# Optimization experiments

Hardware: AMD Instinct MI355X
Metric: run time of the kernel (lower is better)

## Reference

```python
import jax, jax.numpy as jnp
import numpy as np

N_NODES, N_EDGES, N_GRAPHS, NUM_FEATURES, NUM_CLASSES = 100000, 1600000, 512, 128, 10
EPS = 1e-5


def gat_conv(x, W, a_src, a_dst, b, src, dst, heads, out_ch):
    # PyG GATConv: h = xW -> [N,H,C]; per-node scores; leaky_relu; segment softmax over dst; scatter-add
    N = x.shape[0]
    h = (x @ W).reshape(N, heads, out_ch)
    s_src = jnp.einsum('nhc,hc->nh', h, a_src)
    s_dst = jnp.einsum('nhc,hc->nh', h, a_dst)
    score = jax.nn.leaky_relu(s_src[src] + s_dst[dst], 0.2)          # [E,H]
    m = jax.ops.segment_max(score, dst, num_segments=N)              # stable softmax per dst node
    e = jnp.exp(score - m[dst])
    denom = jax.ops.segment_sum(e, dst, num_segments=N)
    alpha = e / denom[dst]                                            # self-loops guarantee denom>0
    out = jax.ops.segment_sum(alpha[:, :, None] * h[src], dst, num_segments=N)
    return out.reshape(N, heads * out_ch) + b


def batch_norm(x, g, b):
    mu = x.mean(0)
    var = x.var(0)  # biased, as torch BN uses for normalization
    return g * (x - mu) * jax.lax.rsqrt(var + EPS) + b


def setup_inputs() -> dict:
    key = jax.random.key(0)
    ks = jax.random.split(key, 32)
    r = lambda i, shape: jax.random.normal(ks[i], shape, dtype=jnp.float32) * 0.1
    inp = {
        'x': jax.random.normal(ks[0], (N_NODES, NUM_FEATURES), dtype=jnp.float32),
        'edge_index': jax.random.randint(ks[1], (2, N_EDGES), 0, N_NODES, dtype=jnp.int64),
        'batch': jnp.sort(jax.random.randint(ks[2], (N_NODES,), 0, N_GRAPHS, dtype=jnp.int64)),
        # conv1: 128 -> 8 ch x 8 heads
        'W1': r(3, (NUM_FEATURES, 64)), 'a1s': r(4, (8, 8)), 'a1d': r(5, (8, 8)), 'b1': r(6, (64,)),
        'g1': jnp.ones(64), 'be1': jnp.zeros(64),
        'lW1': r(7, (64, 8)), 'lb1': r(8, (8,)), 'gl1': jnp.ones(8), 'bel1': jnp.zeros(8),
        # conv2: 8 -> 16 ch x 4 heads
        'W2': r(9, (8, 64)), 'a2s': r(10, (4, 16)), 'a2d': r(11, (4, 16)), 'b2': r(12, (64,)),
        'g2': jnp.ones(64), 'be2': jnp.zeros(64),
        'lW2': r(13, (64, 16)), 'lb2': r(14, (16,)), 'gl2': jnp.ones(16), 'bel2': jnp.zeros(16),
        # conv3: 16 -> 24 ch x 4 heads
        'W3': r(15, (16, 96)), 'a3s': r(16, (4, 24)), 'a3d': r(17, (4, 24)), 'b3': r(18, (96,)),
        'g3': jnp.ones(96), 'be3': jnp.zeros(96),
        'oW': r(19, (96, NUM_CLASSES)), 'ob': r(20, (NUM_CLASSES,)),
    }
    return inp


def reference(x, edge_index, batch, W1, a1s, a1d, b1, g1, be1, lW1, lb1, gl1, bel1,
              W2, a2s, a2d, b2, g2, be2, lW2, lb2, gl2, bel2,
              W3, a3s, a3d, b3, g3, be3, oW, ob):
    N = x.shape[0]
    loops = jnp.arange(N, dtype=edge_index.dtype)
    src = jnp.concatenate([edge_index[0], loops])  # PyG add_self_loops default
    dst = jnp.concatenate([edge_index[1], loops])

    h = gat_conv(x, W1, a1s, a1d, b1, src, dst, 8, 8)
    h = jax.nn.relu(batch_norm(h, g1, be1))
    h = jax.nn.relu(batch_norm(h @ lW1 + lb1, gl1, bel1))

    h = gat_conv(h, W2, a2s, a2d, b2, src, dst, 4, 16)
    h = jax.nn.relu(batch_norm(h, g2, be2))
    h = jax.nn.relu(batch_norm(h @ lW2 + lb2, gl2, bel2))

    h = gat_conv(h, W3, a3s, a3d, b3, src, dst, 4, 24)
    h = jax.nn.relu(batch_norm(h, g3, be3))

    sums = jax.ops.segment_sum(h, batch, num_segments=N_GRAPHS)
    cnts = jax.ops.segment_sum(jnp.ones((N,), h.dtype), batch, num_segments=N_GRAPHS)
    pooled = sums / jnp.maximum(cnts, 1.0)[:, None]
    return pooled @ oW + ob
```

## Files before the change

kernel.cpp:

```cpp
#include <hip/hip_runtime.h>
#include <hip/hip_fp16.h>
#include <math.h>

#define NN 100000
#define NE 1600000
#define ET (NE + NN)
#define NG 512
#define STATS_BLOCKS 240
#define SCAN_B 1024
#define SCAN_NB ((NN + SCAN_B - 1) / SCAN_B)
#define PSLOTS (ET + 7 * NN)

#define BSH 9
#define NB  ((NN + 511) / 512)
#define BCAP 12288
#define CHUNK 4096


__global__ __launch_bounds__(256) void part_pass1(const int* __restrict__ ei,
                                                  int* __restrict__ bcur,
                                                  unsigned* __restrict__ pairs) {
    __shared__ unsigned pck[CHUNK];
    __shared__ unsigned ordv[CHUNK];
    __shared__ unsigned char bkt[CHUNK];
    __shared__ unsigned char obkt[CHUNK];
    __shared__ int hist[NB + 1];
    __shared__ int lofs[NB + 1];
    __shared__ int cur[NB + 1];
    __shared__ int gpos[NB];
    __shared__ int lh[256];

    int t = threadIdx.x;
    int base = blockIdx.x * CHUNK;
    for (int i = t; i <= NB; i += 256) hist[i] = 0;
    __syncthreads();
    for (int i = t; i < CHUNK; i += 256) {
        int e = base + i;
        int b;
        unsigned p = 0;
        if (e < ET) {
            int s, d;
            if (e < NE) { s = ei[e]; d = ei[NE + e]; }
            else        { s = d = e - NE; }
            b = d >> BSH;
            p = ((unsigned)s << BSH) | (unsigned)(d & 511);
        } else b = NB;
        bkt[i] = (unsigned char)b;
        pck[i] = p;
        atomicAdd(&hist[b], 1);
    }
    __syncthreads();
    int v = (t <= NB) ? hist[t] : 0;
    lh[t] = v;
    __syncthreads();
    for (int off = 1; off < 256; off <<= 1) {
        int x = (t >= off) ? lh[t - off] : 0;
        __syncthreads();
        lh[t] += x;
        __syncthreads();
    }
    if (t <= NB) { lofs[t] = lh[t] - v; cur[t] = lh[t] - v; }
    __syncthreads();
    if (t < NB) {
        int h = hist[t];
        gpos[t] = (h > 0) ? atomicAdd(&bcur[t], h) : 0;
    }
    __syncthreads();
    for (int i = t; i < CHUNK; i += 256) {
        int b = bkt[i];
        int pos = atomicAdd(&cur[b], 1);
        ordv[pos] = pck[i];
        obkt[pos] = (unsigned char)b;
    }
    __syncthreads();
    int nvalid = lofs[NB];
    for (int i = t; i < nvalid; i += 256) {
        int b = obkt[i];
        int dst = gpos[b] + (i - lofs[b]);
        if (dst < BCAP) pairs[(size_t)b * BCAP + dst] = ordv[i];
    }
}


__global__ __launch_bounds__(256) void bucket_counts(const unsigned* __restrict__ pairs,
                                                     const int* __restrict__ bcur,
                                                     int* __restrict__ counts) {
    __shared__ int lhist[512];
    int b = blockIdx.x;
    int t = threadIdx.x;
    for (int i = t; i < 512; i += 256) lhist[i] = 0;
    __syncthreads();
    int cnt = min(bcur[b], BCAP);
    const unsigned* seg = pairs + (size_t)b * BCAP;
    for (int i = t; i < cnt; i += 256)
        atomicAdd(&lhist[seg[i] & 511], 1);
    __syncthreads();
    int nbase = b << BSH;
    for (int i = t; i < 512; i += 256) {
        int n = nbase + i;
        if (n < NN) counts[n] = lhist[i];
    }
}


__global__ __launch_bounds__(256) void bucket_scatter(const unsigned* __restrict__ pairs,
                                                      const int* __restrict__ bcur,
                                                      const int* __restrict__ offsets,
                                                      int* __restrict__ srcs) {
    __shared__ int cur[512];
    int b = blockIdx.x;
    int t = threadIdx.x;
    int nbase = b << BSH;
    for (int i = t; i < 512; i += 256) {
        int n = nbase + i;
        cur[i] = (n < NN) ? offsets[n] : 0;
    }
    __syncthreads();
    int cnt = min(bcur[b], BCAP);
    const unsigned* seg = pairs + (size_t)b * BCAP;
    for (int i = t; i < cnt; i += 256) {
        unsigned p = seg[i];
        int pos = atomicAdd(&cur[p & 511], 1);
        srcs[pos] = (int)(p >> BSH);
    }
}


__global__ void graph_bounds(const int* __restrict__ batch, int* __restrict__ goff) {
    int g = blockIdx.x * blockDim.x + threadIdx.x;
    if (g > NG) return;
    int lo = 0, hi = NN;
    while (lo < hi) {
        int mid = (lo + hi) >> 1;
        if (batch[mid] < g) lo = mid + 1; else hi = mid;
    }
    goff[g] = lo;
}


__global__ void scan_reduce(const int* __restrict__ in, int* __restrict__ bsum) {
    __shared__ int lds[256];
    int b = blockIdx.x, t = threadIdx.x;
    int s = 0;
    for (int i = t; i < SCAN_B; i += 256) {
        int idx = b * SCAN_B + i;
        if (idx < NN) s += (in[idx] + 7) & ~7;
    }
    lds[t] = s;
    __syncthreads();
    for (int off = 128; off > 0; off >>= 1) {
        if (t < off) lds[t] += lds[t + off];
        __syncthreads();
    }
    if (t == 0) bsum[b] = lds[0];
}

__global__ void scan_bsums(const int* __restrict__ bsum, int nb, int* __restrict__ boff,
                           int* __restrict__ total_loc) {
    __shared__ int lds[128];
    int t = threadIdx.x;
    int v = (t < nb) ? bsum[t] : 0;
    lds[t] = v;
    __syncthreads();
    for (int off = 1; off < 128; off <<= 1) {
        int x = (t >= off) ? lds[t - off] : 0;
        __syncthreads();
        lds[t] += x;
        __syncthreads();
    }
    if (t < nb) boff[t] = lds[t] - v;
    if (t == nb - 1) {
        boff[nb] = lds[t];
        if (total_loc) *total_loc = lds[t];
    }
}

__global__ void scan_final(const int* __restrict__ in, const int* __restrict__ boff,
                           int* __restrict__ out) {
    __shared__ int lds[SCAN_B];
    int b = blockIdx.x, t = threadIdx.x;
    int idx = b * SCAN_B + t;
    int v = (idx < NN) ? ((in[idx] + 7) & ~7) : 0;
    lds[t] = v;
    __syncthreads();
    for (int off = 1; off < SCAN_B; off <<= 1) {
        int x = (t >= off) ? lds[t - off] : 0;
        __syncthreads();
        lds[t] += x;
        __syncthreads();
    }
    if (idx < NN) out[idx] = boff[b] + lds[t] - v;
}


__global__ __launch_bounds__(256) void gemm1(const float* __restrict__ X,
                                             const float* __restrict__ W,
                                             const float* __restrict__ a_s,
                                             const float* __restrict__ a_d,
                                             __half* __restrict__ Hh,
                                             float* __restrict__ SS,
                                             float* __restrict__ SD) {
    __shared__ float wl[128 * 64];
    __shared__ float xl[32 * 132];
    int t = threadIdx.x;
    int n0 = blockIdx.x * 32;
    for (int i = t * 4; i < 128 * 64; i += 1024)
        *(float4*)&wl[i] = *(const float4*)&W[i];
    for (int i = t * 4; i < 32 * 128; i += 1024) {
        int r = i >> 7, c = i & 127;
        int n = n0 + r;
        float4 v = (n < NN) ? *(const float4*)&X[(size_t)n * 128 + c] : make_float4(0, 0, 0, 0);
        *(float4*)&xl[r * 132 + c] = v;
    }
    __syncthreads();
    int cg = (t & 15) * 4;
    int ng = (t >> 4) * 2;
    float acc[2][4] = {};
    for (int k = 0; k < 128; ++k) {
        float4 w4 = *(float4*)&wl[k * 64 + cg];
        #pragma unroll
        for (int j = 0; j < 2; ++j) {
            float xv = xl[(ng + j) * 132 + k];
            acc[j][0] += xv * w4.x; acc[j][1] += xv * w4.y;
            acc[j][2] += xv * w4.z; acc[j][3] += xv * w4.w;
        }
    }
    int hd = cg >> 3;
    int half = cg & 7;
    #pragma unroll
    for (int j = 0; j < 2; ++j) {
        int n = n0 + ng + j;
        float p1 = 0.f, p2 = 0.f;
        #pragma unroll
        for (int k = 0; k < 4; ++k) {
            p1 += acc[j][k] * a_s[hd * 8 + half + k];
            p2 += acc[j][k] * a_d[hd * 8 + half + k];
        }
        float f1 = p1 + __shfl_xor(p1, 1, 64);
        float f2 = p2 + __shfl_xor(p2, 1, 64);
        if (n < NN) {
            __half2 q0 = __floats2half2_rn(acc[j][0], acc[j][1]);
            __half2 q1 = __floats2half2_rn(acc[j][2], acc[j][3]);
            *(__half2*)&Hh[(size_t)n * 64 + cg] = q0;
            *(__half2*)&Hh[(size_t)n * 64 + cg + 2] = q1;
            if (half == 0) {
                SS[(unsigned)n * 8 + hd] = f1;
                SD[(unsigned)n * 8 + hd] = f2;
            }
        }
    }
}


template <int HEADS, int C, int PL, int GRP>
__global__ __launch_bounds__(256) void gat_kernel(const __half* __restrict__ Hh,
                                                  const float* __restrict__ SS,
                                                  const float* __restrict__ SD,
                                                  const int* __restrict__ offsets,
                                                  const int* __restrict__ counts,
                                                  const int* __restrict__ srcs,
                                                  const float* __restrict__ bias,
                                                  __half* __restrict__ GO) {
    constexpr int CH = HEADS * C;
    int wid = blockIdx.x * (blockDim.x >> 6) + (threadIdx.x >> 6);
    int lane = threadIdx.x & 63;
    if (wid >= NN) return;
    int ch0 = lane * PL;
    bool active = ch0 < CH;
    int ch0l = active ? ch0 : 0;
    int head = active ? (ch0 / C) : 0;
    int beg = offsets[wid], end = offsets[wid + 1];
    int deg = counts[wid];
    float sdv = SD[(unsigned)wid * HEADS + head];
    float s = 0.f, a0 = 0.f, a1 = 0.f;
    int e = beg;
    if (GRP == 16) {
        for (; e + 16 <= end; e += 16) {
            int sv[16];
            float wv[16];
            #pragma unroll
            for (int i = 0; i < 16; ++i) {
                sv[i] = srcs[e + i];
                float sc = SS[(unsigned)(sv[i] * HEADS) + head] + sdv;
                sc = fmaxf(sc, 0.f) + 0.2f * fminf(sc, 0.f);
                wv[i] = (e + i - beg) < deg ? __expf(sc) : 0.f;
            }
            float hv0[16];
            #pragma unroll
            for (int i = 0; i < 16; ++i)
                hv0[i] = __half2float(Hh[(unsigned)(sv[i] * CH) + ch0l]);
            float pw[8], pa[8];
            #pragma unroll
            for (int i = 0; i < 8; ++i) {
                pw[i] = wv[2 * i] + wv[2 * i + 1];
                pa[i] = wv[2 * i] * hv0[2 * i] + wv[2 * i + 1] * hv0[2 * i + 1];
            }
            s  += ((pw[0] + pw[1]) + (pw[2] + pw[3])) + ((pw[4] + pw[5]) + (pw[6] + pw[7]));
            a0 += ((pa[0] + pa[1]) + (pa[2] + pa[3])) + ((pa[4] + pa[5]) + (pa[6] + pa[7]));
        }
    }
    for (; e < end; e += 8) {
        int sv[8];
        float wv[8];
        #pragma unroll
        for (int i = 0; i < 8; ++i) {
            sv[i] = srcs[e + i];
            float sc = SS[(unsigned)(sv[i] * HEADS) + head] + sdv;
            sc = fmaxf(sc, 0.f) + 0.2f * fminf(sc, 0.f);
            wv[i] = (e + i - beg) < deg ? __expf(sc) : 0.f;
        }
        float hv0[8], hv1[8];
        #pragma unroll
        for (int i = 0; i < 8; ++i) {
            if (PL == 2) {
                __half2 hp = *(const __half2*)&Hh[(unsigned)(sv[i] * CH) + ch0l];
                hv0[i] = __low2float(hp); hv1[i] = __high2float(hp);
            } else {
                hv0[i] = __half2float(Hh[(unsigned)(sv[i] * CH) + ch0l]);
                hv1[i] = 0.f;
            }
        }
        float ws = ((wv[0] + wv[1]) + (wv[2] + wv[3])) + ((wv[4] + wv[5]) + (wv[6] + wv[7]));
        float as0 = ((wv[0] * hv0[0] + wv[1] * hv0[1]) + (wv[2] * hv0[2] + wv[3] * hv0[3]))
                  + ((wv[4] * hv0[4] + wv[5] * hv0[5]) + (wv[6] * hv0[6] + wv[7] * hv0[7]));
        s += ws;
        a0 += as0;
        if (PL == 2) {
            float as1 = ((wv[0] * hv1[0] + wv[1] * hv1[1]) + (wv[2] * hv1[2] + wv[3] * hv1[3]))
                      + ((wv[4] * hv1[4] + wv[5] * hv1[5]) + (wv[6] * hv1[6] + wv[7] * hv1[7]));
            a1 += as1;
        }
    }
    if (active) {
        float inv = 1.f / s;
        if (PL == 2) {
            *(__half2*)&GO[(unsigned)(wid * CH) + ch0] =
                __floats2half2_rn(a0 * inv + bias[ch0], a1 * inv + bias[ch0 + 1]);
        } else {
            GO[(unsigned)(wid * CH) + ch0] = __float2half(a0 * inv + bias[ch0]);
        }
    }
}


__global__ void stats_kernel(const float* __restrict__ X, int Nn, int C,
                             float* __restrict__ partial) {
    int t = threadIdx.x;
    int c = t % C;
    int grp = t / C;
    int G_ = blockDim.x / C;
    float s = 0.f, q = 0.f;
    for (int n = blockIdx.x * G_ + grp; n < Nn; n += gridDim.x * G_) {
        float v = X[(size_t)n * C + c];
        s += v; q += v * v;
    }
    extern __shared__ float lds[];
    lds[t] = s; lds[blockDim.x + t] = q;
    __syncthreads();
    for (int off = blockDim.x >> 1; off >= C; off >>= 1) {
        if (t < off) {
            lds[t] += lds[t + off];
            lds[blockDim.x + t] += lds[blockDim.x + t + off];
        }
        __syncthreads();
    }
    if (t < C) {
        partial[(size_t)blockIdx.x * 2 * C + t] = lds[t];
        partial[(size_t)blockIdx.x * 2 * C + C + t] = lds[blockDim.x + t];
    }
}

__global__ void stats_h_kernel(const __half* __restrict__ X, int Nn, int C,
                               float* __restrict__ partial) {
    int t = threadIdx.x;
    int c = t % C;
    int grp = t / C;
    int G_ = blockDim.x / C;
    float s = 0.f, q = 0.f;
    for (int n = blockIdx.x * G_ + grp; n < Nn; n += gridDim.x * G_) {
        float v = __half2float(X[(size_t)n * C + c]);
        s += v; q += v * v;
    }
    extern __shared__ float lds[];
    lds[t] = s; lds[blockDim.x + t] = q;
    __syncthreads();
    for (int off = blockDim.x >> 1; off >= C; off >>= 1) {
        if (t < off) {
            lds[t] += lds[t + off];
            lds[blockDim.x + t] += lds[blockDim.x + t + off];
        }
        __syncthreads();
    }
    if (t < C) {
        partial[(size_t)blockIdx.x * 2 * C + t] = lds[t];
        partial[(size_t)blockIdx.x * 2 * C + C + t] = lds[blockDim.x + t];
    }
}

__global__ void bn_finalize(const float* __restrict__ partial, int nb, int C, float invN,
                            const float* __restrict__ g, const float* __restrict__ be,
                            float* __restrict__ scale, float* __restrict__ shift) {
    extern __shared__ float red[];
    int t = threadIdx.x;
    int c = t % C;
    int grp = t / C;
    int G_ = blockDim.x / C;
    float s = 0.f, q = 0.f;
    for (int b = grp; b < nb; b += G_) {
        s += partial[(size_t)b * 2 * C + c];
        q += partial[(size_t)b * 2 * C + C + c];
    }
    red[t] = s; red[blockDim.x + t] = q;
    __syncthreads();
    for (int off = blockDim.x >> 1; off >= C; off >>= 1) {
        if (t < off) {
            red[t] += red[t + off];
            red[blockDim.x + t] += red[blockDim.x + t + off];
        }
        __syncthreads();
    }
    if (t < C) {
        float mean = red[t] * invN;
        float var = fmaxf(red[blockDim.x + t] * invN - mean * mean, 0.f);
        float rs = rsqrtf(var + 1e-5f);
        float sc = g[t] * rs;
        scale[t] = sc;
        shift[t] = be[t] - mean * sc;
    }
}


template <int KOUT>
__global__ __launch_bounds__(256) void bnrelu_linear(const __half* __restrict__ X,
                                                     const float* __restrict__ scale,
                                                     const float* __restrict__ shift,
                                                     const float* __restrict__ Lw,
                                                     const float* __restrict__ lb,
                                                     float* __restrict__ U) {
    __shared__ float tl[64 * 65];
    int t = threadIdx.x;
    int n0 = blockIdx.x * 64;
    for (int i = t * 4; i < 64 * 64; i += 1024) {
        int r = i >> 6, cc = i & 63;
        int n = n0 + r;
        float vv[4] = {0.f, 0.f, 0.f, 0.f};
        if (n < NN) {
            float2 v0 = __half22float2(*(const __half2*)&X[(size_t)n * 64 + cc]);
            float2 v1 = __half22float2(*(const __half2*)&X[(size_t)n * 64 + cc + 2]);
            vv[0] = v0.x; vv[1] = v0.y; vv[2] = v1.x; vv[3] = v1.y;
        }
        #pragma unroll
        for (int j = 0; j < 4; ++j)
            tl[r * 65 + cc + j] = fmaxf(vv[j] * scale[cc + j] + shift[cc + j], 0.f);
    }
    __syncthreads();
    int nl = t & 63;
    int kg = (t >> 6) * (KOUT / 4);
    float acc[KOUT / 4] = {};
    for (int l = 0; l < 64; ++l) {
        float v = tl[nl * 65 + l];
        #pragma unroll
        for (int j = 0; j < KOUT / 4; ++j) acc[j] += v * Lw[l * KOUT + kg + j];
    }
    int n = n0 + nl;
    if (n < NN)
        #pragma unroll
        for (int j = 0; j < KOUT / 4; ++j)
            U[(size_t)n * KOUT + kg + j] = acc[j] + lb[kg + j];
}


template <int CIN, int COUT, int H, int C>
__global__ __launch_bounds__(256) void bnrelu_gemm(const float* __restrict__ U,
                                                   const float* __restrict__ scale,
                                                   const float* __restrict__ shift,
                                                   const float* __restrict__ W,
                                                   const float* __restrict__ a_s,
                                                   const float* __restrict__ a_d,
                                                   __half* __restrict__ Hh,
                                                   float* __restrict__ SS,
                                                   float* __restrict__ SD) {
    static_assert(COUT / 4 == C && H == 4, "thread-per-head mapping");
    int t = threadIdx.x;
    int nl = t >> 2;
    int q = t & 3;
    int n = blockIdx.x * 64 + nl;
    if (n >= NN) return;
    constexpr int CPT = COUT / 4;
    float v[CIN];
    #pragma unroll
    for (int c = 0; c < CIN; ++c)
        v[c] = fmaxf(U[(size_t)n * CIN + c] * scale[c] + shift[c], 0.f);
    float acc[CPT] = {};
    #pragma unroll
    for (int c = 0; c < CIN; ++c) {
        #pragma unroll
        for (int j = 0; j < CPT; ++j) acc[j] += v[c] * W[c * COUT + q * CPT + j];
    }
    float s1 = 0.f, s2 = 0.f;
    #pragma unroll
    for (int j = 0; j < CPT; ++j) {
        s1 += acc[j] * a_s[q * C + j];
        s2 += acc[j] * a_d[q * C + j];
    }
    SS[(unsigned)n * H + q] = s1;
    SD[(unsigned)n * H + q] = s2;
    #pragma unroll
    for (int j = 0; j < CPT; j += 2)
        *(__half2*)&Hh[(size_t)n * COUT + q * CPT + j] = __floats2half2_rn(acc[j], acc[j + 1]);
}


__global__ __launch_bounds__(256) void pool_kernel(const __half* __restrict__ GO,
                                                   const float* __restrict__ scale,
                                                   const float* __restrict__ shift,
                                                   const int* __restrict__ goff,
                                                   float* __restrict__ pooled) {
    __shared__ float red[8][32];
    int g = blockIdx.x;
    int ch = blockIdx.y * 32 + (threadIdx.x & 31);
    int row = threadIdx.x >> 5;
    int beg = goff[g], end = goff[g + 1];
    float sc = scale[ch], sh = shift[ch];
    float s = 0.f;
    for (int n = beg + row; n < end; n += 8)
        s += fmaxf(__half2float(GO[(size_t)n * 96 + ch]) * sc + sh, 0.f);
    red[row][threadIdx.x & 31] = s;
    __syncthreads();
    if (row == 0) {
        #pragma unroll
        for (int r = 1; r < 8; ++r) s += red[r][threadIdx.x & 31];
        float cnt = (float)(end - beg);
        pooled[g * 96 + ch] = s / fmaxf(cnt, 1.f);
    }
}

__global__ void final_gemm(const float* __restrict__ pooled, const float* __restrict__ oW,
                           const float* __restrict__ ob, float* __restrict__ out) {
    int idx = blockIdx.x * blockDim.x + threadIdx.x;
    if (idx >= NG * 10) return;
    int g = idx / 10, k = idx % 10;
    float s = ob[k];
    for (int c = 0; c < 96; ++c) s += pooled[g * 96 + c] * oW[c * 10 + k];
    out[idx] = s;
}


extern "C" void kernel_launch(void* const* d_in, const int* in_sizes, int n_in,
                              void* d_out, int out_size, void* d_ws, size_t ws_size,
                              hipStream_t stream) {
    const float* x   = (const float*)d_in[0];
    const int*   ei  = (const int*)d_in[1];
    const int*   bat = (const int*)d_in[2];
    const float *W1 = (const float*)d_in[3], *a1s = (const float*)d_in[4],
                *a1d = (const float*)d_in[5], *b1 = (const float*)d_in[6],
                *g1 = (const float*)d_in[7], *be1 = (const float*)d_in[8],
                *lW1 = (const float*)d_in[9], *lb1 = (const float*)d_in[10],
                *gl1 = (const float*)d_in[11], *bel1 = (const float*)d_in[12],
                *W2 = (const float*)d_in[13], *a2s = (const float*)d_in[14],
                *a2d = (const float*)d_in[15], *b2 = (const float*)d_in[16],
                *g2 = (const float*)d_in[17], *be2 = (const float*)d_in[18],
                *lW2 = (const float*)d_in[19], *lb2 = (const float*)d_in[20],
                *gl2 = (const float*)d_in[21], *bel2 = (const float*)d_in[22],
                *W3 = (const float*)d_in[23], *a3s = (const float*)d_in[24],
                *a3d = (const float*)d_in[25], *b3 = (const float*)d_in[26],
                *g3 = (const float*)d_in[27], *be3 = (const float*)d_in[28],
                *oW = (const float*)d_in[29], *ob = (const float*)d_in[30];
    float* out = (float*)d_out;

    int* iw      = (int*)d_ws;
    int* bcur    = iw;
    int* counts  = bcur + NB;
    int* offsets = counts + NN;
    int* goff    = offsets + NN + 1;
    int* bsum    = goff + NG + 1;
    int* boff    = bsum + SCAN_NB;
    int* srcs    = boff + SCAN_NB + 1;
    float* fw      = (float*)(srcs + PSLOTS);
    __half* GOh    = (__half*)fw;
    float* Ub      = fw + (size_t)NN * 96;
    float* SSb     = Ub + (size_t)NN * 16;
    float* SDb     = SSb + (size_t)NN * 8;
    float* partial = SDb + (size_t)NN * 8;
    float* scaleA  = partial + STATS_BLOCKS * 192;
    float* shiftA  = scaleA + 96;
    float* scaleB  = shiftA + 96;
    float* shiftB  = scaleB + 16;
    float* pooled  = shiftB + 16;
    __half* Hh     = (__half*)(pooled + NG * 96);
    unsigned* pairs = (unsigned*)GOh;

    const float invN = 1.0f / (float)NN;

    hipMemsetAsync(bcur, 0, NB * sizeof(int), stream);
    hipMemsetAsync(srcs, 0, (size_t)PSLOTS * sizeof(int), stream);
    part_pass1<<<(ET + CHUNK - 1) / CHUNK, 256, 0, stream>>>(ei, bcur, pairs);
    graph_bounds<<<3, 256, 0, stream>>>(bat, goff);
    bucket_counts<<<NB, 256, 0, stream>>>(pairs, bcur, counts);
    scan_reduce<<<SCAN_NB, 256, 0, stream>>>(counts, bsum);
    scan_bsums<<<1, 128, 0, stream>>>(bsum, SCAN_NB, boff, &offsets[NN]);
    scan_final<<<SCAN_NB, SCAN_B, 0, stream>>>(counts, boff, offsets);
    bucket_scatter<<<NB, 256, 0, stream>>>(pairs, bcur, offsets, srcs);

    gemm1<<<(NN + 31) / 32, 256, 0, stream>>>(x, W1, a1s, a1d, Hh, SSb, SDb);
    gat_kernel<8, 8, 1, 16><<<(NN + 3) / 4, 256, 0, stream>>>(Hh, SSb, SDb, offsets, counts, srcs, b1, GOh);
    stats_h_kernel<<<STATS_BLOCKS, 256, 2 * 256 * sizeof(float), stream>>>(GOh, NN, 64, partial);
    bn_finalize<<<1, 512, 2 * 512 * sizeof(float), stream>>>(partial, STATS_BLOCKS, 64, invN, g1, be1, scaleA, shiftA);
    bnrelu_linear<8><<<(NN + 63) / 64, 256, 0, stream>>>(GOh, scaleA, shiftA, lW1, lb1, Ub);
    stats_kernel<<<STATS_BLOCKS, 256, 2 * 256 * sizeof(float), stream>>>(Ub, NN, 8, partial);
    bn_finalize<<<1, 512, 2 * 512 * sizeof(float), stream>>>(partial, STATS_BLOCKS, 8, invN, gl1, bel1, scaleB, shiftB);

    bnrelu_gemm<8, 64, 4, 16><<<(NN + 63) / 64, 256, 0, stream>>>(Ub, scaleB, shiftB, W2, a2s, a2d, Hh, SSb, SDb);
    gat_kernel<4, 16, 1, 16><<<(NN + 3) / 4, 256, 0, stream>>>(Hh, SSb, SDb, offsets, counts, srcs, b2, GOh);
    stats_h_kernel<<<STATS_BLOCKS, 256, 2 * 256 * sizeof(float), stream>>>(GOh, NN, 64, partial);
    bn_finalize<<<1, 512, 2 * 512 * sizeof(float), stream>>>(partial, STATS_BLOCKS, 64, invN, g2, be2, scaleA, shiftA);
    bnrelu_linear<16><<<(NN + 63) / 64, 256, 0, stream>>>(GOh, scaleA, shiftA, lW2, lb2, Ub);
    stats_kernel<<<STATS_BLOCKS, 256, 2 * 256 * sizeof(float), stream>>>(Ub, NN, 16, partial);
    bn_finalize<<<1, 512, 2 * 512 * sizeof(float), stream>>>(partial, STATS_BLOCKS, 16, invN, gl2, bel2, scaleB, shiftB);

    bnrelu_gemm<16, 96, 4, 24><<<(NN + 63) / 64, 256, 0, stream>>>(Ub, scaleB, shiftB, W3, a3s, a3d, Hh, SSb, SDb);
    gat_kernel<4, 24, 2, 8><<<(NN + 3) / 4, 256, 0, stream>>>(Hh, SSb, SDb, offsets, counts, srcs, b3, GOh);
    stats_h_kernel<<<STATS_BLOCKS, 192, 2 * 192 * sizeof(float), stream>>>(GOh, NN, 96, partial);
    bn_finalize<<<1, 768, 2 * 768 * sizeof(float), stream>>>(partial, STATS_BLOCKS, 96, invN, g3, be3, scaleA, shiftA);

    pool_kernel<<<dim3(NG, 3), 256, 0, stream>>>(GOh, scaleA, shiftA, goff, pooled);
    final_gemm<<<(NG * 10 + 255) / 256, 256, 0, stream>>>(pooled, oW, ob, out);
}
```

Measured before the change: 607.4 us.

## Distribute edge score computation across lanes and broadcast via shuffles in GAT kernel

Rewrites the GAT aggregation loop so that each lane computes the attention score and exp for one (edge, head) pair, then broadcasts source indices and weights to the channel lanes of that head with wavefront shuffles. Before, every lane recomputed scores for all edges in the group. This removes redundant SS loads and exp work per lane, at the cost of many shuffle instructions. Layer 1 drops from a group size of 16 to 8 so that 8 heads by 8 edges fill the 64 lanes. The index padding slots grow by 16, presumably so grouped reads past a segment end stay in bounds.

```diff
diff --git a/kernel.cpp b/kernel.cpp
--- a/kernel.cpp
+++ b/kernel.cpp
@@ -9,7 +9,7 @@
 #define STATS_BLOCKS 240
 #define SCAN_B 1024
 #define SCAN_NB ((NN + SCAN_B - 1) / SCAN_B)
-#define PSLOTS (ET + 7 * NN)
+#define PSLOTS (ET + 7 * NN + 16)
 
 #define BSH 9
 #define NB  ((NN + 511) / 512)
@@ -262,6 +262,7 @@
                                                   const float* __restrict__ bias,
                                                   __half* __restrict__ GO) {
     constexpr int CH = HEADS * C;
+    constexpr int LG = (GRP == 16) ? 4 : 3;
     int wid = blockIdx.x * (blockDim.x >> 6) + (threadIdx.x >> 6);
     int lane = threadIdx.x & 63;
     if (wid >= NN) return;
@@ -269,66 +270,66 @@
     bool active = ch0 < CH;
     int ch0l = active ? ch0 : 0;
     int head = active ? (ch0 / C) : 0;
+    int headGRP = head * GRP;
     int beg = offsets[wid], end = offsets[wid + 1];
     int deg = counts[wid];
-    float sdv = SD[(unsigned)wid * HEADS + head];
+    int sEdge = lane & (GRP - 1);
+    int sHead = (lane >> LG) & (HEADS - 1);
+    float sdvS = SD[(unsigned)wid * HEADS + sHead];
     float s = 0.f, a0 = 0.f, a1 = 0.f;
-    int e = beg;
-    if (GRP == 16) {
-        for (; e + 16 <= end; e += 16) {
-            int sv[16];
-            float wv[16];
+    for (int e = beg; e < end; e += GRP) {
+        int myIdx = e + sEdge;
+        int mySrc = srcs[myIdx];
+        float sc = SS[(unsigned)mySrc * HEADS + sHead] + sdvS;
+        sc = fmaxf(sc, 0.f) + 0.2f * fminf(sc, 0.f);
+        float myW = (myIdx - beg) < deg ? __expf(sc) : 0.f;
+        int sv[GRP];
+        float wv[GRP];
+        #pragma unroll
+        for (int i = 0; i < GRP; ++i) {
+            sv[i] = __shfl(mySrc, headGRP + i, 64);
+            wv[i] = __shfl(myW, headGRP + i, 64);
+        }
+        if (PL == 1) {
+            float hv[GRP];
             #pragma unroll
-            for (int i = 0; i < 16; ++i) {
-                sv[i] = srcs[e + i];
-                float sc = SS[(unsigned)(sv[i] * HEADS) + head] + sdv;
-                sc = fmaxf(sc, 0.f) + 0.2f * fminf(sc, 0.f);
-                wv[i] = (e + i - beg) < deg ? __expf(sc) : 0.f;
+            for (int i = 0; i < GRP; ++i)
+                hv[i] = __half2float(Hh[(unsigned)(sv[i] * CH) + ch0l]);
+            float pw[GRP / 2], pa[GRP / 2];
+            #pragma unroll
+            for (int i = 0; i < GRP / 2; ++i) {
+                pw[i] = wv[2 * i] + wv[2 * i + 1];
+                pa[i] = wv[2 * i] * hv[2 * i] + wv[2 * i + 1] * hv[2 * i + 1];
             }
-            float hv0[16];
             #pragma unroll
-            for (int i = 0; i < 16; ++i)
-                hv0[i] = __half2float(Hh[(unsigned)(sv[i] * CH) + ch0l]);
-            float pw[8], pa[8];
+            for (int st = GRP / 4; st >= 1; st >>= 1) {
+                #pragma unroll
+                for (int i = 0; i < st; ++i) { pw[i] += pw[i + st]; pa[i] += pa[i + st]; }
+            }
+            s += pw[0];
+            a0 += pa[0];
+        } else {
+            float hv0[GRP], hv1[GRP];
             #pragma unroll
-            for (int i = 0; i < 8; ++i) {
+            for (int i = 0; i < GRP; ++i) {
+                __half2 hp = *(const __half2*)&Hh[(unsigned)(sv[i] * CH) + ch0l];
+                hv0[i] = __low2float(hp); hv1[i] = __high2float(hp);
+            }
+            float pw[GRP / 2], pa[GRP / 2], pb[GRP / 2];
+            #pragma unroll
+            for (int i = 0; i < GRP / 2; ++i) {
                 pw[i] = wv[2 * i] + wv[2 * i + 1];
                 pa[i] = wv[2 * i] * hv0[2 * i] + wv[2 * i + 1] * hv0[2 * i + 1];
+                pb[i] = wv[2 * i] * hv1[2 * i] + wv[2 * i + 1] * hv1[2 * i + 1];
             }
-            s  += ((pw[0] + pw[1]) + (pw[2] + pw[3])) + ((pw[4] + pw[5]) + (pw[6] + pw[7]));
-            a0 += ((pa[0] + pa[1]) + (pa[2] + pa[3])) + ((pa[4] + pa[5]) + (pa[6] + pa[7]));
-        }
-    }
-    for (; e < end; e += 8) {
-        int sv[8];
-        float wv[8];
-        #pragma unroll
-        for (int i = 0; i < 8; ++i) {
-            sv[i] = srcs[e + i];
-            float sc = SS[(unsigned)(sv[i] * HEADS) + head] + sdv;
-            sc = fmaxf(sc, 0.f) + 0.2f * fminf(sc, 0.f);
-            wv[i] = (e + i - beg) < deg ? __expf(sc) : 0.f;
-        }
-        float hv0[8], hv1[8];
-        #pragma unroll
-        for (int i = 0; i < 8; ++i) {
-            if (PL == 2) {
-                __half2 hp = *(const __half2*)&Hh[(unsigned)(sv[i] * CH) + ch0l];
-                hv0[i] = __low2float(hp); hv1[i] = __high2float(hp);
-            } else {
-                hv0[i] = __half2float(Hh[(unsigned)(sv[i] * CH) + ch0l]);
-                hv1[i] = 0.f;
+            #pragma unroll
+            for (int st = GRP / 4; st >= 1; st >>= 1) {
+                #pragma unroll
+                for (int i = 0; i < st; ++i) { pw[i] += pw[i + st]; pa[i] += pa[i + st]; pb[i] += pb[i + st]; }
             }
-        }
-        float ws = ((wv[0] + wv[1]) + (wv[2] + wv[3])) + ((wv[4] + wv[5]) + (wv[6] + wv[7]));
-        float as0 = ((wv[0] * hv0[0] + wv[1] * hv0[1]) + (wv[2] * hv0[2] + wv[3] * hv0[3]))
-                  + ((wv[4] * hv0[4] + wv[5] * hv0[5]) + (wv[6] * hv0[6] + wv[7] * hv0[7]));
-        s += ws;
-        a0 += as0;
-        if (PL == 2) {
-            float as1 = ((wv[0] * hv1[0] + wv[1] * hv1[1]) + (wv[2] * hv1[2] + wv[3] * hv1[3]))
-                      + ((wv[4] * hv1[4] + wv[5] * hv1[5]) + (wv[6] * hv1[6] + wv[7] * hv1[7]));
-            a1 += as1;
+            s += pw[0];
+            a0 += pa[0];
+            a1 += pb[0];
         }
     }
     if (active) {
@@ -603,7 +604,7 @@
     bucket_scatter<<<NB, 256, 0, stream>>>(pairs, bcur, offsets, srcs);
 
     gemm1<<<(NN + 31) / 32, 256, 0, stream>>>(x, W1, a1s, a1d, Hh, SSb, SDb);
-    gat_kernel<8, 8, 1, 16><<<(NN + 3) / 4, 256, 0, stream>>>(Hh, SSb, SDb, offsets, counts, srcs, b1, GOh);
+    gat_kernel<8, 8, 1, 8><<<(NN + 3) / 4, 256, 0, stream>>>(Hh, SSb, SDb, offsets, counts, srcs, b1, GOh);
     stats_h_kernel<<<STATS_BLOCKS, 256, 2 * 256 * sizeof(float), stream>>>(GOh, NN, 64, partial);
     bn_finalize<<<1, 512, 2 * 512 * sizeof(float), stream>>>(partial, STATS_BLOCKS, 64, invN, g1, be1, scaleA, shiftA);
     bnrelu_linear<8><<<(NN + 63) / 64, 256, 0, stream>>>(GOh, scaleA, shiftA, lW1, lb1, Ub);
```

After: 610.6 us. About the same (+0.5%).
